# Kernel tuning notes

Measured on AMD Instinct MI355X. Metric: run time of the kernel, lower is better.

The kernel has to match this reference:

```python
import jax, jax.numpy as jnp
import numpy as np

N = 50000
E = 600000
D_IN = 128
D_HID = 128
D_OUT = 40
BN_EPS = 1e-5


def setup_inputs() -> dict:
    key = jax.random.key(0)
    ks = jax.random.split(key, 16)
    g = lambda k, *s: (jax.random.normal(k, s, jnp.float32) * 0.05)
    return {
        "x": jax.random.normal(ks[0], (N, D_IN), jnp.float32),
        "edge_index": jax.random.randint(ks[1], (2, E), 0, N, dtype=jnp.int64),
        "W0": g(ks[2], D_IN, D_HID), "b0": jnp.zeros((D_HID,), jnp.float32),
        "W1": g(ks[3], D_HID, D_HID), "b1": jnp.zeros((D_HID,), jnp.float32),
        "W2": g(ks[4], D_HID, D_OUT), "b2": jnp.zeros((D_OUT,), jnp.float32),
        "g0": 1.0 + g(ks[5], D_HID), "be0": g(ks[6], D_HID),
        "m0": g(ks[7], D_HID), "v0": 0.5 + jax.random.uniform(ks[8], (D_HID,), jnp.float32),
        "g1": 1.0 + g(ks[9], D_HID), "be1": g(ks[10], D_HID),
        "m1": g(ks[11], D_HID), "v1": 0.5 + jax.random.uniform(ks[12], (D_HID,), jnp.float32),
    }


def reference(x, edge_index, W0, b0, W1, b1, W2, b2,
              g0, be0, m0, v0, g1, be1, m1, v1):
    n = x.shape[0]
    loop = jnp.arange(n, dtype=edge_index.dtype)
    # GCN with self-loops: A_hat = A + I, symmetric normalization
    src = jnp.concatenate([edge_index[0], loop])
    dst = jnp.concatenate([edge_index[1], loop])
    deg = jax.ops.segment_sum(jnp.ones_like(dst, jnp.float32), dst, num_segments=n)
    dinv = jax.lax.rsqrt(jnp.maximum(deg, 1.0))
    norm = dinv[src] * dinv[dst]  # [E+N]

    def conv(h, W, b):
        h = h @ W + b                                   # [N, d_out]
        msg = norm[:, None] * h[src]                    # gather + scale
        return jax.ops.segment_sum(msg, dst, num_segments=n)

    def bn_relu(h, g, be, m, v):
        return jax.nn.relu((h - m) * (g * jax.lax.rsqrt(v + BN_EPS)) + be)

    h = bn_relu(conv(x, W0, b0), g0, be0, m0, v0)
    h = bn_relu(conv(h, W1, b1), g1, be1, m1, v1)
    h = conv(h, W2, b2)
    return jax.nn.log_softmax(h, axis=-1)
```

## Files before the change

### kernel.cpp

```cpp
#include <hip/hip_runtime.h>
#include <math.h>

#define BN_EPS 1e-5f
#define CAP 96

typedef unsigned short ushort_t;
typedef __attribute__((ext_vector_type(8))) short short8;
typedef __attribute__((ext_vector_type(4))) float floatx4;

__device__ inline ushort_t f2b(float f) {
    unsigned u = __float_as_uint(f);
    unsigned r = u + 0x7FFFu + ((u >> 16) & 1u);
    return (ushort_t)(r >> 16);
}
__device__ inline float b2f(ushort_t b) { return __uint_as_float(((unsigned)b) << 16); }
__device__ inline float2 u2f2(unsigned u) {
    return make_float2(b2f((ushort_t)(u & 0xffffu)), b2f((ushort_t)(u >> 16)));
}

__device__ inline void cast_weights(const float* __restrict__ W0, const float* __restrict__ W1,
                                    const float* __restrict__ W2, ushort_t* __restrict__ Wt0,
                                    ushort_t* __restrict__ Wt1, ushort_t* __restrict__ Wt2,
                                    int i) {
    if (i < 16384) {
        int nn = i >> 7, k = i & 127;
        Wt0[i] = f2b(W0[k * 128 + nn]);
    } else if (i < 32768) {
        int j = i - 16384;
        int nn = j >> 7, k = j & 127;
        Wt1[j] = f2b(W1[k * 128 + nn]);
    } else if (i < 40960) {
        int j = i - 32768;
        int nn = j >> 7, k = j & 127;
        Wt2[j] = (nn < 40) ? f2b(W2[k * 40 + nn]) : (ushort_t)0;
    }
}

__global__ __launch_bounds__(256) void k_fill_cast(
    const int* __restrict__ ei, int* __restrict__ cnt, ushort_t* __restrict__ ell,
    const float* __restrict__ W0, const float* __restrict__ W1, const float* __restrict__ W2,
    ushort_t* __restrict__ Wt0, ushort_t* __restrict__ Wt1, ushort_t* __restrict__ Wt2,
    int E, int FB)
{
    int bid = blockIdx.x;
    if (bid < FB) {
        int e = bid * 256 + threadIdx.x;
        if (e < E) {
            int s = ei[e];
            int d = ei[E + e];
            int p = atomicAdd(&cnt[d], 1);
            if (p < CAP) ell[(size_t)d * CAP + p] = (ushort_t)s;
        }
        return;
    }
    cast_weights(W0, W1, W2, Wt0, Wt1, Wt2, (bid - FB) * 256 + threadIdx.x);
}

template<int NT, bool AF32>
__global__ __launch_bounds__(256) void k_gemm(const void* __restrict__ Av,
                                              const ushort_t* __restrict__ Wt,
                                              const float* __restrict__ bias,
                                              const int* __restrict__ cnt,
                                              ushort_t* __restrict__ C,
                                              int M, int ncols) {
    __shared__ ushort_t Ws[NT * 128];
    const int tid = threadIdx.x;
    const int ntiles = (M + 127) >> 7;
    const int wave = tid >> 6, lane = tid & 63;
    const int m = lane & 15, quad = lane >> 4;
    constexpr int CT = NT / 16;
    const int r0 = wave * 32;

    for (int t = blockIdx.x; t < ntiles; t += gridDim.x) {
        const int rbase = t << 7;
#pragma unroll
        for (int p = 0; p < NT / 16; ++p) {
            int cid = p * 256 + tid;
            int nr = cid >> 4, seg = cid & 15;
            *(uint4*)(Ws + nr * 128 + ((seg ^ (nr & 15)) << 3)) =
                *(const uint4*)(Wt + (size_t)cid * 8);
        }
        __syncthreads();

        floatx4 acc[2][CT];
#pragma unroll
        for (int rt = 0; rt < 2; ++rt)
#pragma unroll
            for (int ct = 0; ct < CT; ++ct) acc[rt][ct] = (floatx4){0.f, 0.f, 0.f, 0.f};

        const int ra = rbase + r0 + m;
        const int rb = ra + 16;
        const bool oka = ra < M, okb = rb < M;

#pragma unroll
        for (int ks = 0; ks < 4; ++ks) {
            int ko = ks * 32 + quad * 8;
            short8 a0 = {0, 0, 0, 0, 0, 0, 0, 0}, a1 = a0;
            if (AF32) {
                const float* A32 = (const float*)Av;
                if (oka) {
                    const float* p = A32 + (size_t)ra * 128 + ko;
                    float4 f0 = *(const float4*)p, f1 = *(const float4*)(p + 4);
                    a0[0] = f2b(f0.x); a0[1] = f2b(f0.y); a0[2] = f2b(f0.z); a0[3] = f2b(f0.w);
                    a0[4] = f2b(f1.x); a0[5] = f2b(f1.y); a0[6] = f2b(f1.z); a0[7] = f2b(f1.w);
                }
                if (okb) {
                    const float* p = A32 + (size_t)rb * 128 + ko;
                    float4 f0 = *(const float4*)p, f1 = *(const float4*)(p + 4);
                    a1[0] = f2b(f0.x); a1[1] = f2b(f0.y); a1[2] = f2b(f0.z); a1[3] = f2b(f0.w);
                    a1[4] = f2b(f1.x); a1[5] = f2b(f1.y); a1[6] = f2b(f1.z); a1[7] = f2b(f1.w);
                }
            } else {
                const ushort_t* A16 = (const ushort_t*)Av;
                if (oka) a0 = *(const short8*)(A16 + (size_t)ra * 128 + ko);
                if (okb) a1 = *(const short8*)(A16 + (size_t)rb * 128 + ko);
            }
#pragma unroll
            for (int ct = 0; ct < CT; ++ct) {
                short8 b = *(const short8*)(Ws + (ct * 16 + m) * 128 + (((ks * 4 + quad) ^ m) << 3));
                acc[0][ct] = __builtin_amdgcn_mfma_f32_16x16x32_bf16(a0, b, acc[0][ct], 0, 0, 0);
                acc[1][ct] = __builtin_amdgcn_mfma_f32_16x16x32_bf16(a1, b, acc[1][ct], 0, 0, 0);
            }
        }

        float dsc[2][4];
#pragma unroll
        for (int rt = 0; rt < 2; ++rt)
#pragma unroll
            for (int r = 0; r < 4; ++r) {
                int gr = rbase + r0 + rt * 16 + quad * 4 + r;
                dsc[rt][r] = (gr < M) ? rsqrtf((float)(cnt[gr] + 1)) : 0.f;
            }

        __syncthreads();
        constexpr int SEGN = NT / 8, CMASK = SEGN - 1;
#pragma unroll
        for (int rt = 0; rt < 2; ++rt)
#pragma unroll
            for (int ct = 0; ct < CT; ++ct) {
                int col = ct * 16 + m;
                float bv = (col < ncols) ? bias[col] : 0.f;
                int seg = col >> 3, cl = col & 7;
#pragma unroll
                for (int r = 0; r < 4; ++r) {
                    int row = r0 + rt * 16 + quad * 4 + r;
                    Ws[row * NT + ((seg ^ (row & CMASK)) << 3) + cl] =
                        f2b((acc[rt][ct][r] + bv) * dsc[rt][r]);
                }
            }
        __syncthreads();
        constexpr int CPT = (128 * SEGN) / 256;
#pragma unroll
        for (int p = 0; p < CPT; ++p) {
            int cid = p * 256 + tid;
            int row = cid / SEGN, seg = cid & CMASK;
            int gr = rbase + row;
            if (gr < M)
                *(uint4*)(C + (size_t)gr * NT + seg * 8) =
                    *(const uint4*)(Ws + row * NT + ((seg ^ (row & CMASK)) << 3));
        }
        __syncthreads();
    }
}

__global__ __launch_bounds__(256) void agg128_sliced(
    const ushort_t* __restrict__ h,
    const int* __restrict__ cnt,
    const ushort_t* __restrict__ ell,
    const float* __restrict__ g, const float* __restrict__ be,
    const float* __restrict__ mB, const float* __restrict__ v,
    ushort_t* __restrict__ out, int n)
{
    const int bid = blockIdx.x;
    const int slice = bid & 3;
    const int tid = threadIdx.x;
    const int wave = tid >> 6, lane = tid & 63;
    const int quad = lane >> 4, l16 = lane & 15;
    const int r = ((bid >> 2) << 4) + wave * 4 + quad;
    if (r >= n) return;
    const int so = slice << 4;
    const unsigned* h2 = (const unsigned*)h;

    const int c0 = (slice << 5) + l16 * 2;
    const float s0f = g[c0] * rsqrtf(v[c0] + BN_EPS);
    const float s1f = g[c0 + 1] * rsqrtf(v[c0 + 1] + BN_EPS);
    const float m0v = mB[c0], m1v = mB[c0 + 1], b0v = be[c0], b1v = be[c0 + 1];

    int cd = cnt[r];
    float dv = rsqrtf((float)(cd + 1));
    float2 hv = u2f2(h2[(size_t)r * 64 + so + l16]);
    float ax = hv.x, ay = hv.y;
    int c = min(cd, CAP);
    const ushort_t* row = ell + (size_t)r * CAP;
    int k = 0;
    for (; k + 8 <= c; k += 8) {
        uint4 iv = *(const uint4*)(row + k);
        int s[8] = {(int)(iv.x & 0xffffu), (int)(iv.x >> 16),
                    (int)(iv.y & 0xffffu), (int)(iv.y >> 16),
                    (int)(iv.z & 0xffffu), (int)(iv.z >> 16),
                    (int)(iv.w & 0xffffu), (int)(iv.w >> 16)};
#pragma unroll
        for (int j = 0; j < 8; ++j) {
            float2 t = u2f2(h2[(size_t)s[j] * 64 + so + l16]);
            ax += t.x;
            ay += t.y;
        }
    }
    if (k < c) {
        int rem = c - k;
        uint4 iv = *(const uint4*)(row + k);
        int sr[8] = {(int)(iv.x & 0xffffu), (int)(iv.x >> 16),
                     (int)(iv.y & 0xffffu), (int)(iv.y >> 16),
                     (int)(iv.z & 0xffffu), (int)(iv.z >> 16),
                     (int)(iv.w & 0xffffu), (int)(iv.w >> 16)};
        int s[8];
#pragma unroll
        for (int j = 0; j < 8; ++j) s[j] = (j < rem) ? sr[j] : 0;
#pragma unroll
        for (int j = 0; j < 8; ++j) {
            float2 t = u2f2(h2[(size_t)s[j] * 64 + so + l16]);
            ax += (j < rem) ? t.x : 0.f;
            ay += (j < rem) ? t.y : 0.f;
        }
    }
    ax *= dv;
    ay *= dv;
    float o0 = fmaxf(fmaf(ax - m0v, s0f, b0v), 0.f);
    float o1 = fmaxf(fmaf(ay - m1v, s1f, b1v), 0.f);
    unsigned ov = (unsigned)f2b(o0) | ((unsigned)f2b(o1) << 16);
    ((unsigned*)out)[(size_t)r * 64 + so + l16] = ov;
}

__global__ __launch_bounds__(256) void k_agg40(const ushort_t* __restrict__ h,
                                               const int* __restrict__ cnt,
                                               const ushort_t* __restrict__ ell,
                                               float* __restrict__ out, int n) {
    int wv = __builtin_amdgcn_readfirstlane((blockIdx.x * 256 + threadIdx.x) >> 6);
    int lane = threadIdx.x & 63;
    if (wv >= n) return;
    int cd = cnt[wv];
    float dv = rsqrtf((float)(cd + 1));
    float acc = b2f(h[(size_t)wv * 64 + lane]);
    int c = min(cd, CAP);
    const ushort_t* row = ell + (size_t)wv * CAP;
    int k = 0;
    for (; k + 8 <= c; k += 8) {
        int s[8];
#pragma unroll
        for (int j = 0; j < 8; ++j) s[j] = row[k + j];
#pragma unroll
        for (int j = 0; j < 8; ++j) acc += b2f(h[(size_t)s[j] * 64 + lane]);
    }
    if (k < c) {
        int rem = c - k;
        int s[8];
#pragma unroll
        for (int j = 0; j < 8; ++j) {
            int sr = row[k + j];
            s[j] = (j < rem) ? sr : 0;
        }
#pragma unroll
        for (int j = 0; j < 8; ++j) {
            float t = b2f(h[(size_t)s[j] * 64 + lane]);
            acc += (j < rem) ? t : 0.f;
        }
    }
    acc *= dv;
    bool act = lane < 40;
    float xv = act ? acc : -INFINITY;
    float mx = xv;
#pragma unroll
    for (int off = 32; off > 0; off >>= 1) mx = fmaxf(mx, __shfl_xor(mx, off, 64));
    float ex = act ? expf(acc - mx) : 0.f;
    float se = ex;
#pragma unroll
    for (int off = 32; off > 0; off >>= 1) se += __shfl_xor(se, off, 64);
    float r = acc - mx - logf(se);
    if (act) out[(size_t)wv * 40 + lane] = r;
}


extern "C" void kernel_launch(void* const* d_in, const int* in_sizes, int n_in,
                              void* d_out, int out_size, void* d_ws, size_t ws_size,
                              hipStream_t stream) {
    const float* x = (const float*)d_in[0];
    const int* ei = (const int*)d_in[1];
    const float* W0 = (const float*)d_in[2];
    const float* b0 = (const float*)d_in[3];
    const float* W1 = (const float*)d_in[4];
    const float* b1 = (const float*)d_in[5];
    const float* W2 = (const float*)d_in[6];
    const float* b2 = (const float*)d_in[7];
    const float* g0 = (const float*)d_in[8];
    const float* be0 = (const float*)d_in[9];
    const float* m0 = (const float*)d_in[10];
    const float* v0 = (const float*)d_in[11];
    const float* g1 = (const float*)d_in[12];
    const float* be1 = (const float*)d_in[13];
    const float* m1 = (const float*)d_in[14];
    const float* v1 = (const float*)d_in[15];
    float* out = (float*)d_out;

    const int N = in_sizes[0] / 128;
    const int E = in_sizes[1] / 2;

    char* wp = (char*)d_ws;
    auto alloc = [&](size_t bytes) -> char* {
        char* p = wp;
        wp += (bytes + 255) & ~(size_t)255;
        return p;
    };
    int* cnt = (int*)alloc((size_t)N * 4);
    ushort_t* ell = (ushort_t*)alloc(((size_t)N * CAP + 16) * 2);
    ushort_t* hA = (ushort_t*)alloc((size_t)N * 128 * 2);
    ushort_t* hB = (ushort_t*)alloc((size_t)N * 128 * 2);
    ushort_t* hA2 = (ushort_t*)alloc((size_t)N * 128 * 2);
    ushort_t* hB2 = (ushort_t*)alloc((size_t)N * 128 * 2);
    ushort_t* hL = (ushort_t*)alloc((size_t)N * 64 * 2);
    ushort_t* Wt0 = (ushort_t*)alloc(128 * 128 * 2);
    ushort_t* Wt1 = (ushort_t*)alloc(128 * 128 * 2);
    ushort_t* Wt2 = (ushort_t*)alloc(64 * 128 * 2);

    const int GB = (N + 127) / 128;
    const int AG = 4 * ((N + 15) / 16);
    const int FB = (E + 255) / 256;
    const int CB = 160;

    hipMemsetAsync(cnt, 0, (size_t)N * 4, stream);
    k_fill_cast<<<FB + CB, 256, 0, stream>>>(ei, cnt, ell, W0, W1, W2,
                                             Wt0, Wt1, Wt2, E, FB);
    k_gemm<128, true><<<GB, 256, 0, stream>>>(x, Wt0, b0, cnt, hA, N, 128);
    agg128_sliced<<<AG, 256, 0, stream>>>(hA, cnt, ell, g0, be0, m0, v0, hB, N);
    k_gemm<128, false><<<GB, 256, 0, stream>>>(hB, Wt1, b1, cnt, hA2, N, 128);
    agg128_sliced<<<AG, 256, 0, stream>>>(hA2, cnt, ell, g1, be1, m1, v1, hB2, N);
    k_gemm<64, false><<<GB, 256, 0, stream>>>(hB2, Wt2, b2, cnt, hL, N, 40);
    k_agg40<<<(N + 3) / 4, 256, 0, stream>>>(hL, cnt, ell, out, N);
}
```

Baseline: 252.3 us.

## Aggregate full 128-wide rows per wave and pack two rows per wave in final layer

The 128-wide aggregation changes from four column-sliced blocks per 16 rows to one wave per destination row, with each lane gathering a 32-bit bf16 pair. Each neighbor gather is now one contiguous 256-byte row read, and the row's index list is read once instead of once per slice. The 40-wide final aggregation packs two rows per wave, each half-wave gathering 64-wide padded rows as bf16 pairs and writing float2 outputs. This halves the number of waves in that kernel and avoids idle padding lanes. In exchange, the BN parameters are loaded per thread at the end, and the per-row wave assignment reduces parallelism per row.

```diff
diff --git a/kernel.cpp b/kernel.cpp
--- a/kernel.cpp
+++ b/kernel.cpp
@@ -163,52 +163,41 @@
     }
 }
 
-__global__ __launch_bounds__(256) void agg128_sliced(
-    const ushort_t* __restrict__ h,
-    const int* __restrict__ cnt,
-    const ushort_t* __restrict__ ell,
-    const float* __restrict__ g, const float* __restrict__ be,
-    const float* __restrict__ mB, const float* __restrict__ v,
-    ushort_t* __restrict__ out, int n)
-{
-    const int bid = blockIdx.x;
-    const int slice = bid & 3;
-    const int tid = threadIdx.x;
-    const int wave = tid >> 6, lane = tid & 63;
-    const int quad = lane >> 4, l16 = lane & 15;
-    const int r = ((bid >> 2) << 4) + wave * 4 + quad;
-    if (r >= n) return;
-    const int so = slice << 4;
+__global__ __launch_bounds__(256) void agg128_bn(const ushort_t* __restrict__ h,
+                                                 const int* __restrict__ cnt,
+                                                 const ushort_t* __restrict__ ell,
+                                                 const float* __restrict__ g,
+                                                 const float* __restrict__ be,
+                                                 const float* __restrict__ mB,
+                                                 const float* __restrict__ v,
+                                                 ushort_t* __restrict__ out, int n) {
+    int wv = __builtin_amdgcn_readfirstlane((blockIdx.x * 256 + threadIdx.x) >> 6);
+    int lane = threadIdx.x & 63;
+    if (wv >= n) return;
     const unsigned* h2 = (const unsigned*)h;
-
-    const int c0 = (slice << 5) + l16 * 2;
-    const float s0f = g[c0] * rsqrtf(v[c0] + BN_EPS);
-    const float s1f = g[c0 + 1] * rsqrtf(v[c0 + 1] + BN_EPS);
-    const float m0v = mB[c0], m1v = mB[c0 + 1], b0v = be[c0], b1v = be[c0 + 1];
-
-    int cd = cnt[r];
+    int cd = cnt[wv];
     float dv = rsqrtf((float)(cd + 1));
-    float2 hv = u2f2(h2[(size_t)r * 64 + so + l16]);
+    float2 hv = u2f2(h2[(size_t)wv * 64 + lane]);
     float ax = hv.x, ay = hv.y;
     int c = min(cd, CAP);
-    const ushort_t* row = ell + (size_t)r * CAP;
+    const uint4* rowv = (const uint4*)(ell + (size_t)wv * CAP);
     int k = 0;
     for (; k + 8 <= c; k += 8) {
-        uint4 iv = *(const uint4*)(row + k);
+        uint4 iv = rowv[k >> 3];
         int s[8] = {(int)(iv.x & 0xffffu), (int)(iv.x >> 16),
                     (int)(iv.y & 0xffffu), (int)(iv.y >> 16),
                     (int)(iv.z & 0xffffu), (int)(iv.z >> 16),
                     (int)(iv.w & 0xffffu), (int)(iv.w >> 16)};
 #pragma unroll
         for (int j = 0; j < 8; ++j) {
-            float2 t = u2f2(h2[(size_t)s[j] * 64 + so + l16]);
+            float2 t = u2f2(h2[(size_t)s[j] * 64 + lane]);
             ax += t.x;
             ay += t.y;
         }
     }
     if (k < c) {
         int rem = c - k;
-        uint4 iv = *(const uint4*)(row + k);
+        uint4 iv = rowv[k >> 3];
         int sr[8] = {(int)(iv.x & 0xffffu), (int)(iv.x >> 16),
                      (int)(iv.y & 0xffffu), (int)(iv.y >> 16),
                      (int)(iv.z & 0xffffu), (int)(iv.z >> 16),
@@ -218,65 +207,88 @@
         for (int j = 0; j < 8; ++j) s[j] = (j < rem) ? sr[j] : 0;
 #pragma unroll
         for (int j = 0; j < 8; ++j) {
-            float2 t = u2f2(h2[(size_t)s[j] * 64 + so + l16]);
+            float2 t = u2f2(h2[(size_t)s[j] * 64 + lane]);
             ax += (j < rem) ? t.x : 0.f;
             ay += (j < rem) ? t.y : 0.f;
         }
     }
     ax *= dv;
     ay *= dv;
-    float o0 = fmaxf(fmaf(ax - m0v, s0f, b0v), 0.f);
-    float o1 = fmaxf(fmaf(ay - m1v, s1f, b1v), 0.f);
+    int c0 = lane * 2;
+    float s0f = g[c0] * rsqrtf(v[c0] + BN_EPS);
+    float s1f = g[c0 + 1] * rsqrtf(v[c0 + 1] + BN_EPS);
+    float o0 = fmaxf(fmaf(ax - mB[c0], s0f, be[c0]), 0.f);
+    float o1 = fmaxf(fmaf(ay - mB[c0 + 1], s1f, be[c0 + 1]), 0.f);
     unsigned ov = (unsigned)f2b(o0) | ((unsigned)f2b(o1) << 16);
-    ((unsigned*)out)[(size_t)r * 64 + so + l16] = ov;
+    ((unsigned*)out)[(size_t)wv * 64 + lane] = ov;
 }
 
 __global__ __launch_bounds__(256) void k_agg40(const ushort_t* __restrict__ h,
                                                const int* __restrict__ cnt,
                                                const ushort_t* __restrict__ ell,
                                                float* __restrict__ out, int n) {
-    int wv = __builtin_amdgcn_readfirstlane((blockIdx.x * 256 + threadIdx.x) >> 6);
-    int lane = threadIdx.x & 63;
-    if (wv >= n) return;
-    int cd = cnt[wv];
+    const int wslot = (blockIdx.x * 256 + threadIdx.x) >> 6;
+    const int lane = threadIdx.x & 63;
+    const int half = lane >> 5, l = lane & 31;
+    const int r = wslot * 2 + half;
+    const bool ok = r < n;
+    const unsigned* h2 = (const unsigned*)h;
+
+    int cd = ok ? cnt[r] : 0;
     float dv = rsqrtf((float)(cd + 1));
-    float acc = b2f(h[(size_t)wv * 64 + lane]);
-    int c = min(cd, CAP);
-    const ushort_t* row = ell + (size_t)wv * CAP;
+    float a0 = 0.f, a1 = 0.f;
+    if (ok) {
+        float2 hv = u2f2(h2[(size_t)r * 32 + l]);
+        a0 = hv.x; a1 = hv.y;
+    }
+    int c = ok ? min(cd, CAP) : 0;
+    const uint4* rowv = (const uint4*)(ell + (size_t)r * CAP);
     int k = 0;
     for (; k + 8 <= c; k += 8) {
-        int s[8];
-#pragma unroll
-        for (int j = 0; j < 8; ++j) s[j] = row[k + j];
-#pragma unroll
-        for (int j = 0; j < 8; ++j) acc += b2f(h[(size_t)s[j] * 64 + lane]);
+        uint4 iv = rowv[k >> 3];
+        int s[8] = {(int)(iv.x & 0xffffu), (int)(iv.x >> 16),
+                    (int)(iv.y & 0xffffu), (int)(iv.y >> 16),
+                    (int)(iv.z & 0xffffu), (int)(iv.z >> 16),
+                    (int)(iv.w & 0xffffu), (int)(iv.w >> 16)};
+#pragma unroll
+        for (int j = 0; j < 8; ++j) {
+            float2 t = u2f2(h2[(size_t)s[j] * 32 + l]);
+            a0 += t.x;
+            a1 += t.y;
+        }
     }
     if (k < c) {
         int rem = c - k;
+        uint4 iv = rowv[k >> 3];
+        int sr[8] = {(int)(iv.x & 0xffffu), (int)(iv.x >> 16),
+                     (int)(iv.y & 0xffffu), (int)(iv.y >> 16),
+                     (int)(iv.z & 0xffffu), (int)(iv.z >> 16),
+                     (int)(iv.w & 0xffffu), (int)(iv.w >> 16)};
         int s[8];
 #pragma unroll
+        for (int j = 0; j < 8; ++j) s[j] = (j < rem) ? sr[j] : 0;
+#pragma unroll
         for (int j = 0; j < 8; ++j) {
-            int sr = row[k + j];
-            s[j] = (j < rem) ? sr : 0;
-        }
-#pragma unroll
-        for (int j = 0; j < 8; ++j) {
-            float t = b2f(h[(size_t)s[j] * 64 + lane]);
-            acc += (j < rem) ? t : 0.f;
-        }
-    }
-    acc *= dv;
-    bool act = lane < 40;
-    float xv = act ? acc : -INFINITY;
-    float mx = xv;
-#pragma unroll
-    for (int off = 32; off > 0; off >>= 1) mx = fmaxf(mx, __shfl_xor(mx, off, 64));
-    float ex = act ? expf(acc - mx) : 0.f;
+            float2 t = u2f2(h2[(size_t)s[j] * 32 + l]);
+            a0 += (j < rem) ? t.x : 0.f;
+            a1 += (j < rem) ? t.y : 0.f;
+        }
+    }
+    a0 *= dv;
+    a1 *= dv;
+    const bool act = (l < 20) && ok;
+    float mx = act ? fmaxf(a0, a1) : -INFINITY;
+#pragma unroll
+    for (int off = 16; off > 0; off >>= 1) mx = fmaxf(mx, __shfl_xor(mx, off, 32));
+    float ex = act ? (expf(a0 - mx) + expf(a1 - mx)) : 0.f;
     float se = ex;
 #pragma unroll
-    for (int off = 32; off > 0; off >>= 1) se += __shfl_xor(se, off, 64);
-    float r = acc - mx - logf(se);
-    if (act) out[(size_t)wv * 40 + lane] = r;
+    for (int off = 16; off > 0; off >>= 1) se += __shfl_xor(se, off, 32);
+    float ls = logf(se);
+    if (act) {
+        float2 o = make_float2(a0 - mx - ls, a1 - mx - ls);
+        *(float2*)(out + (size_t)r * 40 + 2 * l) = o;
+    }
 }
 
 
@@ -322,7 +334,8 @@
     ushort_t* Wt2 = (ushort_t*)alloc(64 * 128 * 2);
 
     const int GB = (N + 127) / 128;
-    const int AG = 4 * ((N + 15) / 16);
+    const int AB = (N + 3) / 4;
+    const int A4 = ((N + 1) / 2 + 3) / 4;
     const int FB = (E + 255) / 256;
     const int CB = 160;
 
@@ -330,9 +343,9 @@
     k_fill_cast<<<FB + CB, 256, 0, stream>>>(ei, cnt, ell, W0, W1, W2,
                                              Wt0, Wt1, Wt2, E, FB);
     k_gemm<128, true><<<GB, 256, 0, stream>>>(x, Wt0, b0, cnt, hA, N, 128);
-    agg128_sliced<<<AG, 256, 0, stream>>>(hA, cnt, ell, g0, be0, m0, v0, hB, N);
+    agg128_bn<<<AB, 256, 0, stream>>>(hA, cnt, ell, g0, be0, m0, v0, hB, N);
     k_gemm<128, false><<<GB, 256, 0, stream>>>(hB, Wt1, b1, cnt, hA2, N, 128);
-    agg128_sliced<<<AG, 256, 0, stream>>>(hA2, cnt, ell, g1, be1, m1, v1, hB2, N);
+    agg128_bn<<<AB, 256, 0, stream>>>(hA2, cnt, ell, g1, be1, m1, v1, hB2, N);
     k_gemm<64, false><<<GB, 256, 0, stream>>>(hB2, Wt2, b2, cnt, hL, N, 40);
-    k_agg40<<<(N + 3) / 4, 256, 0, stream>>>(hL, cnt, ell, out, N);
-}
+    k_agg40<<<A4, 256, 0, stream>>>(hL, cnt, ell, out, N);
+}
```

After: 228.6 us. 9.4% less time.
